# Optimization experiments

Measured on AMD Instinct MI355X. Metric: run time of the kernel, lower is better.

## Reference

```python
import jax, jax.numpy as jnp
import numpy as np

NEG_SLOPE = 0.2


def gat_conv(feat, src, dst, W, al, ar, num_nodes, activation):
    # feat: [N, F_in]; W: [F_in, H*D]; al, ar: [H, D]
    H, D = al.shape
    h = (feat @ W).reshape(-1, H, D)                      # [N, H, D]
    el = jnp.sum(h * al, axis=-1)                         # [N, H]
    er = jnp.sum(h * ar, axis=-1)                         # [N, H]
    e = jax.nn.leaky_relu(el[src] + er[dst], NEG_SLOPE)   # [E, H]
    # edge softmax over incoming edges of each destination node
    emax = jax.ops.segment_max(e, dst, num_segments=num_nodes)   # [N, H]
    ee = jnp.exp(e - emax[dst])                           # [E, H]
    denom = jax.ops.segment_sum(ee, dst, num_segments=num_nodes)  # [N, H]
    alpha = ee / jnp.maximum(denom[dst], 1e-9)            # [E, H]
    msg = h[src] * alpha[:, :, None]                      # [E, H, D]
    out = jax.ops.segment_sum(msg, dst, num_segments=num_nodes)   # [N, H, D]
    return activation(out) if activation is not None else out


def setup_inputs() -> dict:
    key = jax.random.key(0)
    ks = jax.random.split(key, 12)
    N, E, F_IN, HID, C = 100000, 1600000, 256, 32, 40
    heads = [4, 4, 1]
    inp = {
        "feats": jax.random.normal(ks[0], (N, F_IN), dtype=jnp.float32),
        "src": jax.random.randint(ks[1], (E,), 0, N, dtype=jnp.int32),
        "dst": jax.random.randint(ks[2], (E,), 0, N, dtype=jnp.int32),
    }
    def glorot(k, shape):
        fan = shape[0] + shape[-1]
        return jax.random.normal(k, shape, dtype=jnp.float32) * np.sqrt(2.0 / fan)
    # layer 0: in=256 -> heads[0]*HID
    inp["W0"] = glorot(ks[3], (F_IN, heads[0] * HID))
    inp["al0"] = glorot(ks[4], (heads[0], HID))
    inp["ar0"] = glorot(ks[5], (heads[0], HID))
    # layer 1: in=heads[0]*HID -> heads[1]*HID
    inp["W1"] = glorot(ks[6], (heads[0] * HID, heads[1] * HID))
    inp["al1"] = glorot(ks[7], (heads[1], HID))
    inp["ar1"] = glorot(ks[8], (heads[1], HID))
    # output layer: in=heads[1]*HID -> heads[2]*C
    inp["W2"] = glorot(ks[9], (heads[1] * HID, heads[2] * C))
    inp["al2"] = glorot(ks[10], (heads[2], C))
    inp["ar2"] = glorot(ks[11], (heads[2], C))
    return inp


def reference(feats, src, dst, W0, al0, ar0, W1, al1, ar1, W2, al2, ar2):
    N = feats.shape[0]
    elu = jax.nn.elu
    h1 = gat_conv(feats, src, dst, W0, al0, ar0, N, elu).reshape(N, -1)  # flatten(1)
    h2 = gat_conv(h1, src, dst, W1, al1, ar1, N, elu).reshape(N, -1)
    logits = gat_conv(h2, src, dst, W2, al2, ar2, N, None).mean(axis=1)  # mean over heads
    return (logits, h1, h2)
```

## Files before the change

kernel.cpp:

```cpp
#include <hip/hip_runtime.h>
#include <hip/hip_bf16.h>

#define NEG_SLOPE 0.2f
#define BW 256
#define MAXB 512

typedef __attribute__((ext_vector_type(8))) short short8;
typedef __attribute__((ext_vector_type(4))) float f32x4;

__device__ inline float bf2f(short s) {
    union { unsigned u; float f; } v;
    v.u = ((unsigned)(unsigned short)s) << 16;
    return v.f;
}
__device__ inline short f2bf(float f) {
    __hip_bfloat16 h = __float2bfloat16(f);
    return (short)*reinterpret_cast<unsigned short*>(&h);
}
__device__ inline void gload16(const void* g, void* lds) {
    __builtin_amdgcn_global_load_lds((const __attribute__((address_space(1))) void*)g,
                                     (__attribute__((address_space(3))) void*)lds, 16, 0, 0);
}


__global__ __launch_bounds__(256) void bhist_kernel(const int* __restrict__ dst,
                                                    int* __restrict__ bcnt, int E, int NB) {
    __shared__ int h[MAXB];
    int tid = threadIdx.x;
    for (int i = tid; i < NB; i += 256) h[i] = 0;
    __syncthreads();
    int e0 = blockIdx.x * 4096;
#pragma unroll
    for (int i = 0; i < 16; ++i) {
        int e = e0 + i * 256 + tid;
        if (e < E) atomicAdd(&h[dst[e] >> 8], 1);
    }
    __syncthreads();
    for (int i = tid; i < NB; i += 256)
        if (h[i]) atomicAdd(&bcnt[i], h[i]);
}

__global__ __launch_bounds__(512) void bscan_kernel(const int* __restrict__ bcnt,
                                                    int* __restrict__ bbase,
                                                    int* __restrict__ bcur, int NB, int E) {
    __shared__ int lds[512];
    int tid = threadIdx.x;
    int v = (tid < NB) ? bcnt[tid] : 0;
    lds[tid] = v;
    __syncthreads();
    int x = v;
    for (int off = 1; off < 512; off <<= 1) {
        int y = (tid >= off) ? lds[tid - off] : 0;
        __syncthreads();
        x += y;
        lds[tid] = x;
        __syncthreads();
    }
    int excl = x - v;
    if (tid < NB) {
        bbase[tid] = excl;
        bcur[tid] = excl;
    }
    if (tid == 0) bbase[NB] = E;
}

__global__ __launch_bounds__(256) void bpart_kernel(const int* __restrict__ dst,
                                                    const int* __restrict__ src,
                                                    int* __restrict__ bcur,
                                                    unsigned* __restrict__ tmp, int E, int NB) {
    __shared__ int h[MAXB], h2[MAXB], base[MAXB];
    int tid = threadIdx.x;
    for (int i = tid; i < NB; i += 256) { h[i] = 0; h2[i] = 0; }
    __syncthreads();
    int e0 = blockIdx.x * 4096;
    unsigned pk[16];
    short bb[16];
#pragma unroll
    for (int i = 0; i < 16; ++i) {
        int e = e0 + i * 256 + tid;
        bool valid = e < E;
        int d = valid ? dst[e] : 0;
        int s = valid ? src[e] : 0;
        bb[i] = valid ? (short)(d >> 8) : (short)-1;
        pk[i] = (unsigned)s | ((unsigned)(d & 255) << 17);
        if (valid) atomicAdd(&h[d >> 8], 1);
    }
    __syncthreads();
    for (int i = tid; i < NB; i += 256)
        base[i] = h[i] ? atomicAdd(&bcur[i], h[i]) : 0;
    __syncthreads();
#pragma unroll
    for (int i = 0; i < 16; ++i) {
        if (bb[i] >= 0) {
            int p = base[bb[i]] + atomicAdd(&h2[bb[i]], 1);
            tmp[p] = pk[i];
        }
    }
}

__global__ __launch_bounds__(256) void bsort_kernel(const unsigned* __restrict__ tmp,
                                                    const int* __restrict__ bbase,
                                                    int* __restrict__ csr,
                                                    int* __restrict__ offsets, int N, int NB) {
    __shared__ int cnt[BW], cur[BW];
    int b = blockIdx.x;
    int tid = threadIdx.x;
    int Rb = bbase[b], Rend = bbase[b + 1];
    cnt[tid] = 0;
    __syncthreads();
    for (int i = Rb + tid; i < Rend; i += 256) atomicAdd(&cnt[tmp[i] >> 17], 1);
    __syncthreads();
    int v = cnt[tid];
    cur[tid] = v;
    __syncthreads();
    int x = v;
    for (int off = 1; off < 256; off <<= 1) {
        int y = (tid >= off) ? cur[tid - off] : 0;
        __syncthreads();
        x += y;
        cur[tid] = x;
        __syncthreads();
    }
    int excl = x - v;
    int g = b * BW + tid;
    if (g <= N) offsets[g] = Rb + excl;
    cur[tid] = Rb + excl;
    __syncthreads();
    for (int i = Rb + tid; i < Rend; i += 256) {
        unsigned p = tmp[i];
        int pos = atomicAdd(&cur[p >> 17], 1);
        csr[pos] = (int)(p & 0x1FFFFu);
    }
}


__global__ __launch_bounds__(256) void cvtT_kernel(const float* __restrict__ in,
                                                   __hip_bfloat16* __restrict__ out,
                                                   int K, int Nc) {
    int i = blockIdx.x * 256 + threadIdx.x;
    if (i >= K * Nc) return;
    int k = i / Nc, n = i % Nc;
    out[(size_t)n * K + k] = __float2bfloat16(in[i]);
}


template <bool CVT_A>
__global__ __launch_bounds__(256) void gemm_mfma(const void* __restrict__ Av,
                                                 const __hip_bfloat16* __restrict__ Bt,
                                                 __hip_bfloat16* __restrict__ Cb,
                                                 int M, int K) {
    __shared__ __align__(16) short smem[8192];
    const int tid = threadIdx.x;
    const int lane = tid & 63;
    const int w = tid >> 6;
    const int wr = w >> 1, wc = w & 1;
    const int bm = blockIdx.x * 128;
    f32x4 acc[4][4];
#pragma unroll
    for (int m = 0; m < 4; ++m)
#pragma unroll
        for (int n = 0; n < 4; ++n) acc[m][n] = 0.f;

    for (int k0 = 0; k0 < K; k0 += 32) {
#pragma unroll
        for (int i = 0; i < 2; ++i) {
            const int c = (w * 2 + i) * 64 + lane;
            const int row = c >> 2;
            const int kpg = (c & 3) ^ (row & 3);
            int grow = bm + row;
            grow = grow < M ? grow : M - 1;
            if (CVT_A) {
                const float* gp = (const float*)Av + (size_t)grow * K + k0 + kpg * 8;
                f32x4 f0 = __builtin_nontemporal_load((const f32x4*)gp);
                f32x4 f1 = __builtin_nontemporal_load((const f32x4*)(gp + 4));
                short8 v;
                v[0] = f2bf(f0[0]); v[1] = f2bf(f0[1]); v[2] = f2bf(f0[2]); v[3] = f2bf(f0[3]);
                v[4] = f2bf(f1[0]); v[5] = f2bf(f1[1]); v[6] = f2bf(f1[2]); v[7] = f2bf(f1[3]);
                *(short8*)&smem[c * 8] = v;
            } else {
                const __hip_bfloat16* gp =
                    (const __hip_bfloat16*)Av + (size_t)grow * K + k0 + kpg * 8;
                gload16(gp, &smem[(w * 2 + i) * 512]);
            }
        }
#pragma unroll
        for (int i = 0; i < 2; ++i) {
            const int c = (w * 2 + i) * 64 + lane;
            const int col = c >> 2;
            const int kpg = (c & 3) ^ (col & 3);
            const __hip_bfloat16* gp = Bt + (size_t)col * K + k0 + kpg * 8;
            gload16(gp, &smem[4096 + (w * 2 + i) * 512]);
        }
        __syncthreads();
        short8 a[4], b[4];
        const int kp = lane >> 4;
#pragma unroll
        for (int m = 0; m < 4; ++m) {
            const int row = wr * 64 + m * 16 + (lane & 15);
            a[m] = *(const short8*)&smem[row * 32 + ((kp ^ (row & 3)) << 3)];
        }
#pragma unroll
        for (int n = 0; n < 4; ++n) {
            const int col = wc * 64 + n * 16 + (lane & 15);
            b[n] = *(const short8*)&smem[4096 + col * 32 + ((kp ^ (col & 3)) << 3)];
        }
#pragma unroll
        for (int m = 0; m < 4; ++m)
#pragma unroll
            for (int n = 0; n < 4; ++n)
                acc[m][n] = __builtin_amdgcn_mfma_f32_16x16x32_bf16(a[m], b[n], acc[m][n], 0, 0, 0);
        __syncthreads();
    }
#pragma unroll
    for (int m = 0; m < 4; ++m)
#pragma unroll
        for (int j = 0; j < 4; ++j) {
            int row = bm + wr * 64 + m * 16 + (lane >> 4) * 4 + j;
            if (row >= M) continue;
#pragma unroll
            for (int n = 0; n < 4; ++n) {
                int col = wc * 64 + n * 16 + (lane & 15);
                Cb[(size_t)row * 128 + col] = __float2bfloat16(acc[m][n][j]);
            }
        }
}


__global__ __launch_bounds__(256) void gemm40_kernel(const __hip_bfloat16* __restrict__ A,
                                                     const float* __restrict__ W,
                                                     __hip_bfloat16* __restrict__ C, int M) {
    int rowb = blockIdx.x * 256 + threadIdx.x;
    int row = rowb < M ? rowb : M - 1;
    float acc[40];
#pragma unroll
    for (int c = 0; c < 40; ++c) acc[c] = 0.f;
    const short8* ap = (const short8*)(A + (size_t)row * 128);
#pragma unroll 1
    for (int kc = 0; kc < 16; ++kc) {
        short8 v = ap[kc];
#pragma unroll
        for (int j = 0; j < 8; ++j) {
            float f = bf2f(v[j]);
            const float* wrow = W + (kc * 8 + j) * 40;
#pragma unroll
            for (int c = 0; c < 40; ++c) acc[c] += f * wrow[c];
        }
    }
    if (rowb < M) {
#pragma unroll
        for (int c = 0; c < 40; ++c) C[(size_t)rowb * 64 + c] = __float2bfloat16(acc[c]);
#pragma unroll
        for (int c = 40; c < 64; ++c) C[(size_t)rowb * 64 + c] = __float2bfloat16(0.f);
    }
}


__global__ __launch_bounds__(256) void eler4_kernel(const __hip_bfloat16* __restrict__ h,
                                                    const float* __restrict__ al,
                                                    const float* __restrict__ ar,
                                                    float* __restrict__ el,
                                                    float* __restrict__ er, int NH) {
    int idx = blockIdx.x * 256 + threadIdx.x;
    if (idx >= NH) return;
    int hh = idx & 3;
    const short8* hp = (const short8*)(h + (size_t)idx * 32);
    float sl = 0.f, sr = 0.f;
#pragma unroll
    for (int ck = 0; ck < 4; ++ck) {
        short8 v = hp[ck];
#pragma unroll
        for (int j = 0; j < 8; ++j) {
            float f = bf2f(v[j]);
            sl += f * al[hh * 32 + ck * 8 + j];
            sr += f * ar[hh * 32 + ck * 8 + j];
        }
    }
    el[idx] = sl;
    er[idx] = sr;
}

__global__ __launch_bounds__(256) void eler1_kernel(const __hip_bfloat16* __restrict__ h,
                                                    const float* __restrict__ al,
                                                    const float* __restrict__ ar,
                                                    float* __restrict__ el,
                                                    float* __restrict__ er, int N) {
    int idx = blockIdx.x * 256 + threadIdx.x;
    if (idx >= N) return;
    const __hip_bfloat162* hp = (const __hip_bfloat162*)(h + (size_t)idx * 64);
    float sl = 0.f, sr = 0.f;
#pragma unroll
    for (int d = 0; d < 20; ++d) {
        float2 f = __bfloat1622float2(hp[d]);
        sl += f.x * al[d * 2] + f.y * al[d * 2 + 1];
        sr += f.x * ar[d * 2] + f.y * ar[d * 2 + 1];
    }
    el[idx] = sl;
    er[idx] = sr;
}


__global__ __launch_bounds__(256) void gat_agg4_kernel(
    const int* __restrict__ offsets, const int* __restrict__ csr_src,
    const float* __restrict__ el, const float* __restrict__ er,
    const __hip_bfloat16* __restrict__ hfeat, float* __restrict__ outf,
    unsigned* __restrict__ outb, int N) {
    int node = blockIdx.x * 4 + (threadIdx.x >> 6);
    if (node >= N) return;
    int lane = threadIdx.x & 63;
    int ha = lane & 3;
    int es = lane >> 2;
    int cl = lane & 31;
    int half = lane >> 5;
    int h2 = cl >> 3;
    int beg = offsets[node], end = offsets[node + 1];
    float ern = er[node * 4 + ha];
    float m_run = -1e30f, d_run = 0.f;
    float acc[4] = {0.f, 0.f, 0.f, 0.f};
    const __hip_bfloat16* hcol = hfeat + cl * 4;
    for (int base = beg; base < end; base += 16) {
        int b = base + es;
        bool valid = b < end;
        int s = valid ? csr_src[b] : 0;
        float x = -1e30f;
        if (valid) {
            x = el[s * 4 + ha] + ern;
            x = x > 0.f ? x : NEG_SLOPE * x;
        }
        float cm = x;
        cm = fmaxf(cm, __shfl_xor(cm, 4));
        cm = fmaxf(cm, __shfl_xor(cm, 8));
        cm = fmaxf(cm, __shfl_xor(cm, 16));
        cm = fmaxf(cm, __shfl_xor(cm, 32));
        float m_new = fmaxf(m_run, cm);
        float scale = __expf(m_run - m_new);
        m_run = m_new;
        float p = valid ? __expf(x - m_new) : 0.f;
        float cs = p;
        cs += __shfl_xor(cs, 4);
        cs += __shfl_xor(cs, 8);
        cs += __shfl_xor(cs, 16);
        cs += __shfl_xor(cs, 32);
        d_run = d_run * scale + cs;
        float scl2 = __shfl(scale, h2);
        acc[0] *= scl2; acc[1] *= scl2; acc[2] *= scl2; acc[3] *= scl2;
        int cnt = min(16, end - base);
        float av[8];
        int rv[8];
#pragma unroll
        for (int k = 0; k < 8; ++k) {
            int e = half + 2 * k;
            float a = __shfl(p, (e << 2) | h2);
            rv[k] = __shfl(s, e << 2);
            av[k] = (e < cnt) ? a : 0.f;
        }
        ushort4 hv[8];
#pragma unroll
        for (int k = 0; k < 8; ++k)
            hv[k] = *(const ushort4*)(hcol + (size_t)rv[k] * 128);
#pragma unroll
        for (int k = 0; k < 8; ++k) {
            acc[0] += bf2f((short)hv[k].x) * av[k];
            acc[1] += bf2f((short)hv[k].y) * av[k];
            acc[2] += bf2f((short)hv[k].z) * av[k];
            acc[3] += bf2f((short)hv[k].w) * av[k];
        }
    }
#pragma unroll
    for (int j = 0; j < 4; ++j) acc[j] += __shfl_xor(acc[j], 32);
    float idn = 1.f / fmaxf(__shfl(d_run, h2), 1e-9f);
    if (half == 0) {
        float v[4];
#pragma unroll
        for (int j = 0; j < 4; ++j) {
            float t = acc[j] * idn;
            v[j] = t > 0.f ? t : __expf(t) - 1.f;
        }
        f32x4 fo = {v[0], v[1], v[2], v[3]};
        *(f32x4*)(outf + (size_t)node * 128 + cl * 4) = fo;
        unsigned u0 = (unsigned short)f2bf(v[0]) | ((unsigned)(unsigned short)f2bf(v[1]) << 16);
        unsigned u1 = (unsigned short)f2bf(v[2]) | ((unsigned)(unsigned short)f2bf(v[3]) << 16);
        uint2 uo = {u0, u1};
        *(uint2*)(outb + (size_t)node * 64 + cl * 2) = uo;
    }
}


__global__ __launch_bounds__(256) void gat_agg1_kernel(
    const int* __restrict__ offsets, const int* __restrict__ csr_src,
    const float* __restrict__ el, const float* __restrict__ er,
    const __hip_bfloat16* __restrict__ hfeat, float* __restrict__ logits, int N) {
    int node = blockIdx.x * 4 + (threadIdx.x >> 6);
    if (node >= N) return;
    int lane = threadIdx.x & 63;
    int cl = lane & 31;
    int half = lane >> 5;
    int beg = offsets[node], end = offsets[node + 1];
    float ern = er[node];
    float m_run = -1e30f, d_run = 0.f;
    float acc0 = 0.f, acc1 = 0.f;
    const __hip_bfloat16* hcol = hfeat + cl * 2;
    for (int base = beg; base < end; base += 64) {
        int b = base + lane;
        bool valid = b < end;
        int s = valid ? csr_src[b] : 0;
        float x = -1e30f;
        if (valid) {
            x = el[s] + ern;
            x = x > 0.f ? x : NEG_SLOPE * x;
        }
        float cm = x;
#pragma unroll
        for (int off = 1; off < 64; off <<= 1) cm = fmaxf(cm, __shfl_xor(cm, off));
        float m_new = fmaxf(m_run, cm);
        float scale = __expf(m_run - m_new);
        m_run = m_new;
        float p = valid ? __expf(x - m_new) : 0.f;
        float cs = p;
#pragma unroll
        for (int off = 1; off < 64; off <<= 1) cs += __shfl_xor(cs, off);
        d_run = d_run * scale + cs;
        acc0 *= scale; acc1 *= scale;
        int cnt = min(64, end - base);
        for (int sb = 0; sb < cnt; sb += 16) {
            float av[8];
            int rv[8];
#pragma unroll
            for (int k = 0; k < 8; ++k) {
                int e = sb + half + 2 * k;
                float a = __shfl(p, e & 63);
                rv[k] = __shfl(s, e & 63);
                av[k] = (e < cnt) ? a : 0.f;
            }
            unsigned hv[8];
#pragma unroll
            for (int k = 0; k < 8; ++k)
                hv[k] = *(const unsigned*)(hcol + (size_t)rv[k] * 64);
#pragma unroll
            for (int k = 0; k < 8; ++k) {
                acc0 += bf2f((short)(hv[k] & 0xFFFF)) * av[k];
                acc1 += bf2f((short)(hv[k] >> 16)) * av[k];
            }
        }
    }
    acc0 += __shfl_xor(acc0, 32);
    acc1 += __shfl_xor(acc1, 32);
    float idn = 1.f / fmaxf(d_run, 1e-9f);
    if (half == 0 && cl < 20) {
        float2 fo = {acc0 * idn, acc1 * idn};
        *(float2*)(logits + (size_t)node * 40 + cl * 2) = fo;
    }
}


extern "C" void kernel_launch(void* const* d_in, const int* in_sizes, int n_in,
                              void* d_out, int out_size, void* d_ws, size_t ws_size,
                              hipStream_t stream) {
    const float* feats = (const float*)d_in[0];
    const int* src = (const int*)d_in[1];
    const int* dst = (const int*)d_in[2];
    const float* W0 = (const float*)d_in[3];
    const float* al0 = (const float*)d_in[4];
    const float* ar0 = (const float*)d_in[5];
    const float* W1 = (const float*)d_in[6];
    const float* al1 = (const float*)d_in[7];
    const float* ar1 = (const float*)d_in[8];
    const float* W2 = (const float*)d_in[9];
    const float* al2 = (const float*)d_in[10];
    const float* ar2 = (const float*)d_in[11];

    const int N = in_sizes[0] / 256;
    const int E = in_sizes[1];
    const int NB = (N + BW - 1) / BW;

    float* out = (float*)d_out;
    float* logits = out;
    float* h1 = out + (size_t)N * 40;
    float* h2 = h1 + (size_t)N * 128;

    char* p = (char*)d_ws;
    __hip_bfloat16* hA = (__hip_bfloat16*)p; p += (size_t)N * 128 * 2;
    __hip_bfloat16* hB = (__hip_bfloat16*)p; p += (size_t)N * 128 * 2;
    float* el = (float*)p;   p += (size_t)N * 4 * 4;
    float* er = (float*)p;   p += (size_t)N * 4 * 4;
    __hip_bfloat16* Wt0 = (__hip_bfloat16*)p; p += 128 * 256 * 2;
    __hip_bfloat16* Wt1 = (__hip_bfloat16*)p; p += 128 * 128 * 2;
    int* offsets = (int*)p;  p += (size_t)(N + 1) * 4;
    int* bcnt = (int*)p;     p += MAXB * 4;
    int* bbase = (int*)p;    p += (MAXB + 1) * 4;
    int* bcur = (int*)p;     p += MAXB * 4;
    int* csr = (int*)p;      p += (size_t)E * 4;
    unsigned* tmp = (unsigned*)hA;

    const int gN256 = (N + 255) / 256;
    const int gE4096 = (E + 4095) / 4096;
    const int gM128 = (N + 127) / 128;
    const int gAgg = (N + 3) / 4;

    hipMemsetAsync(bcnt, 0, MAXB * sizeof(int), stream);
    bhist_kernel<<<gE4096, 256, 0, stream>>>(dst, bcnt, E, NB);
    bscan_kernel<<<1, 512, 0, stream>>>(bcnt, bbase, bcur, NB, E);
    bpart_kernel<<<gE4096, 256, 0, stream>>>(dst, src, bcur, tmp, E, NB);
    bsort_kernel<<<NB, 256, 0, stream>>>(tmp, bbase, csr, offsets, N, NB);

    cvtT_kernel<<<(256 * 128 + 255) / 256, 256, 0, stream>>>(W0, Wt0, 256, 128);
    cvtT_kernel<<<(128 * 128 + 255) / 256, 256, 0, stream>>>(W1, Wt1, 128, 128);

    gemm_mfma<true><<<gM128, 256, 0, stream>>>(feats, Wt0, hA, N, 256);
    eler4_kernel<<<(N * 4 + 255) / 256, 256, 0, stream>>>(hA, al0, ar0, el, er, N * 4);
    gat_agg4_kernel<<<gAgg, 256, 0, stream>>>(offsets, csr, el, er, hA, h1, (unsigned*)hB, N);

    gemm_mfma<false><<<gM128, 256, 0, stream>>>(hB, Wt1, hA, N, 128);
    eler4_kernel<<<(N * 4 + 255) / 256, 256, 0, stream>>>(hA, al1, ar1, el, er, N * 4);
    gat_agg4_kernel<<<gAgg, 256, 0, stream>>>(offsets, csr, el, er, hA, h2, (unsigned*)hB, N);

    gemm40_kernel<<<gN256, 256, 0, stream>>>(hB, W2, hA, N);
    eler1_kernel<<<gN256, 256, 0, stream>>>(hA, al2, ar2, el, er, N);
    gat_agg1_kernel<<<gAgg, 256, 0, stream>>>(offsets, csr, el, er, hA, logits, N);
}
```

Before: 407.2 us.

## Pack source index and fp16 weight into one shuffle, fuse small kernels

The aggregation kernels now pack the source node index (17 bits) and an fp16 attention weight into one 32-bit value, so each edge needs one shuffle instead of two. The bf16 unpack uses cheaper bit operations, and inactive lanes in the single-head layer skip their gathers. The two weight-transpose kernels are merged into one launch, and the layer-3 el/er computation is folded into the 40-column GEMM epilogue, removing a kernel and a re-read of h. The trade-off is that attention weights drop from fp32 to 15-bit fp16 precision, and node indices must fit in 17 bits.

```diff
diff --git a/kernel.cpp b/kernel.cpp
--- a/kernel.cpp
+++ b/kernel.cpp
@@ -1,5 +1,6 @@
 #include <hip/hip_runtime.h>
 #include <hip/hip_bf16.h>
+#include <hip/hip_fp16.h>
 
 #define NEG_SLOPE 0.2f
 #define BW 256
@@ -16,6 +17,26 @@
 __device__ inline short f2bf(float f) {
     __hip_bfloat16 h = __float2bfloat16(f);
     return (short)*reinterpret_cast<unsigned short*>(&h);
+}
+__device__ inline float lo_bf(unsigned u) {
+    union { unsigned u; float f; } v;
+    v.u = u << 16;
+    return v.f;
+}
+__device__ inline float hi_bf(unsigned u) {
+    union { unsigned u; float f; } v;
+    v.u = u & 0xFFFF0000u;
+    return v.f;
+}
+__device__ inline unsigned pack_sa(int s, float p) {
+    __half h = __float2half(p);
+    unsigned hb = (unsigned)*reinterpret_cast<unsigned short*>(&h);
+    return ((unsigned)s << 15) | (hb & 0x7FFFu);
+}
+__device__ inline float unpack_a(unsigned u) {
+    unsigned short hb = (unsigned short)(u & 0x7FFFu);
+    __half h = *reinterpret_cast<__half*>(&hb);
+    return __half2float(h);
 }
 __device__ inline void gload16(const void* g, void* lds) {
     __builtin_amdgcn_global_load_lds((const __attribute__((address_space(1))) void*)g,
@@ -134,13 +155,19 @@
 }
 
 
-__global__ __launch_bounds__(256) void cvtT_kernel(const float* __restrict__ in,
-                                                   __hip_bfloat16* __restrict__ out,
-                                                   int K, int Nc) {
+__global__ __launch_bounds__(256) void cvtT2_kernel(const float* __restrict__ W0,
+                                                    __hip_bfloat16* __restrict__ Wt0,
+                                                    const float* __restrict__ W1,
+                                                    __hip_bfloat16* __restrict__ Wt1) {
     int i = blockIdx.x * 256 + threadIdx.x;
-    if (i >= K * Nc) return;
-    int k = i / Nc, n = i % Nc;
-    out[(size_t)n * K + k] = __float2bfloat16(in[i]);
+    if (i < 256 * 128) {
+        int k = i / 128, n = i % 128;
+        Wt0[(size_t)n * 256 + k] = __float2bfloat16(W0[i]);
+    } else if (i < 256 * 128 + 128 * 128) {
+        int j = i - 256 * 128;
+        int k = j / 128, n = j % 128;
+        Wt1[(size_t)n * 128 + k] = __float2bfloat16(W1[j]);
+    }
 }
 
 
@@ -228,7 +255,11 @@
 
 __global__ __launch_bounds__(256) void gemm40_kernel(const __hip_bfloat16* __restrict__ A,
                                                      const float* __restrict__ W,
-                                                     __hip_bfloat16* __restrict__ C, int M) {
+                                                     const float* __restrict__ al,
+                                                     const float* __restrict__ ar,
+                                                     __hip_bfloat16* __restrict__ C,
+                                                     float* __restrict__ el,
+                                                     float* __restrict__ er, int M) {
     int rowb = blockIdx.x * 256 + threadIdx.x;
     int row = rowb < M ? rowb : M - 1;
     float acc[40];
@@ -247,10 +278,19 @@
         }
     }
     if (rowb < M) {
-#pragma unroll
-        for (int c = 0; c < 40; ++c) C[(size_t)rowb * 64 + c] = __float2bfloat16(acc[c]);
+        float sl = 0.f, sr = 0.f;
+#pragma unroll
+        for (int c = 0; c < 40; ++c) {
+            __hip_bfloat16 hb = __float2bfloat16(acc[c]);
+            float hv = __bfloat162float(hb);
+            C[(size_t)rowb * 64 + c] = hb;
+            sl += hv * al[c];
+            sr += hv * ar[c];
+        }
 #pragma unroll
         for (int c = 40; c < 64; ++c) C[(size_t)rowb * 64 + c] = __float2bfloat16(0.f);
+        el[rowb] = sl;
+        er[rowb] = sr;
     }
 }
 
@@ -274,25 +314,6 @@
             sl += f * al[hh * 32 + ck * 8 + j];
             sr += f * ar[hh * 32 + ck * 8 + j];
         }
-    }
-    el[idx] = sl;
-    er[idx] = sr;
-}
-
-__global__ __launch_bounds__(256) void eler1_kernel(const __hip_bfloat16* __restrict__ h,
-                                                    const float* __restrict__ al,
-                                                    const float* __restrict__ ar,
-                                                    float* __restrict__ el,
-                                                    float* __restrict__ er, int N) {
-    int idx = blockIdx.x * 256 + threadIdx.x;
-    if (idx >= N) return;
-    const __hip_bfloat162* hp = (const __hip_bfloat162*)(h + (size_t)idx * 64);
-    float sl = 0.f, sr = 0.f;
-#pragma unroll
-    for (int d = 0; d < 20; ++d) {
-        float2 f = __bfloat1622float2(hp[d]);
-        sl += f.x * al[d * 2] + f.y * al[d * 2 + 1];
-        sr += f.x * ar[d * 2] + f.y * ar[d * 2 + 1];
     }
     el[idx] = sl;
     er[idx] = sr;
@@ -341,28 +362,28 @@
         cs += __shfl_xor(cs, 16);
         cs += __shfl_xor(cs, 32);
         d_run = d_run * scale + cs;
+        unsigned u_mine = pack_sa(s, p);
         float scl2 = __shfl(scale, h2);
         acc[0] *= scl2; acc[1] *= scl2; acc[2] *= scl2; acc[3] *= scl2;
-        int cnt = min(16, end - base);
-        float av[8];
-        int rv[8];
+        unsigned uk[8];
 #pragma unroll
         for (int k = 0; k < 8; ++k) {
             int e = half + 2 * k;
-            float a = __shfl(p, (e << 2) | h2);
-            rv[k] = __shfl(s, e << 2);
-            av[k] = (e < cnt) ? a : 0.f;
+            uk[k] = __shfl(u_mine, (e << 2) | h2);
         }
         ushort4 hv[8];
 #pragma unroll
         for (int k = 0; k < 8; ++k)
-            hv[k] = *(const ushort4*)(hcol + (size_t)rv[k] * 128);
+            hv[k] = *(const ushort4*)(hcol + ((size_t)(uk[k] >> 15)) * 128);
 #pragma unroll
         for (int k = 0; k < 8; ++k) {
-            acc[0] += bf2f((short)hv[k].x) * av[k];
-            acc[1] += bf2f((short)hv[k].y) * av[k];
-            acc[2] += bf2f((short)hv[k].z) * av[k];
-            acc[3] += bf2f((short)hv[k].w) * av[k];
+            float a = unpack_a(uk[k]);
+            unsigned w0 = (unsigned)hv[k].x | ((unsigned)hv[k].y << 16);
+            unsigned w1 = (unsigned)hv[k].z | ((unsigned)hv[k].w << 16);
+            acc[0] += lo_bf(w0) * a;
+            acc[1] += hi_bf(w0) * a;
+            acc[2] += lo_bf(w1) * a;
+            acc[3] += hi_bf(w1) * a;
         }
     }
 #pragma unroll
@@ -394,6 +415,7 @@
     int lane = threadIdx.x & 63;
     int cl = lane & 31;
     int half = lane >> 5;
+    bool active = cl < 20;
     int beg = offsets[node], end = offsets[node + 1];
     float ern = er[node];
     float m_run = -1e30f, d_run = 0.f;
@@ -420,32 +442,32 @@
         for (int off = 1; off < 64; off <<= 1) cs += __shfl_xor(cs, off);
         d_run = d_run * scale + cs;
         acc0 *= scale; acc1 *= scale;
+        unsigned u_mine = pack_sa(s, p);
         int cnt = min(64, end - base);
         for (int sb = 0; sb < cnt; sb += 16) {
-            float av[8];
-            int rv[8];
+            unsigned uk[8];
 #pragma unroll
             for (int k = 0; k < 8; ++k) {
                 int e = sb + half + 2 * k;
-                float a = __shfl(p, e & 63);
-                rv[k] = __shfl(s, e & 63);
-                av[k] = (e < cnt) ? a : 0.f;
+                uk[k] = __shfl(u_mine, e & 63);
+                if (e >= cnt) uk[k] &= ~0x7FFFu;
             }
             unsigned hv[8];
 #pragma unroll
             for (int k = 0; k < 8; ++k)
-                hv[k] = *(const unsigned*)(hcol + (size_t)rv[k] * 64);
+                hv[k] = active ? *(const unsigned*)(hcol + ((size_t)(uk[k] >> 15)) * 64) : 0u;
 #pragma unroll
             for (int k = 0; k < 8; ++k) {
-                acc0 += bf2f((short)(hv[k] & 0xFFFF)) * av[k];
-                acc1 += bf2f((short)(hv[k] >> 16)) * av[k];
+                float a = unpack_a(uk[k]);
+                acc0 += lo_bf(hv[k]) * a;
+                acc1 += hi_bf(hv[k]) * a;
             }
         }
     }
     acc0 += __shfl_xor(acc0, 32);
     acc1 += __shfl_xor(acc1, 32);
     float idn = 1.f / fmaxf(d_run, 1e-9f);
-    if (half == 0 && cl < 20) {
+    if (half == 0 && active) {
         float2 fo = {acc0 * idn, acc1 * idn};
         *(float2*)(logits + (size_t)node * 40 + cl * 2) = fo;
     }
@@ -502,8 +524,7 @@
     bpart_kernel<<<gE4096, 256, 0, stream>>>(dst, src, bcur, tmp, E, NB);
     bsort_kernel<<<NB, 256, 0, stream>>>(tmp, bbase, csr, offsets, N, NB);
 
-    cvtT_kernel<<<(256 * 128 + 255) / 256, 256, 0, stream>>>(W0, Wt0, 256, 128);
-    cvtT_kernel<<<(128 * 128 + 255) / 256, 256, 0, stream>>>(W1, Wt1, 128, 128);
+    cvtT2_kernel<<<(256 * 128 + 128 * 128 + 255) / 256, 256, 0, stream>>>(W0, Wt0, W1, Wt1);
 
     gemm_mfma<true><<<gM128, 256, 0, stream>>>(feats, Wt0, hA, N, 256);
     eler4_kernel<<<(N * 4 + 255) / 256, 256, 0, stream>>>(hA, al0, ar0, el, er, N * 4);
@@ -513,7 +534,6 @@
     eler4_kernel<<<(N * 4 + 255) / 256, 256, 0, stream>>>(hA, al1, ar1, el, er, N * 4);
     gat_agg4_kernel<<<gAgg, 256, 0, stream>>>(offsets, csr, el, er, hA, h2, (unsigned*)hB, N);
 
-    gemm40_kernel<<<gN256, 256, 0, stream>>>(hB, W2, hA, N);
-    eler1_kernel<<<gN256, 256, 0, stream>>>(hA, al2, ar2, el, er, N);
+    gemm40_kernel<<<gN256, 256, 0, stream>>>(hB, W2, al2, ar2, hA, el, er, N);
     gat_agg1_kernel<<<gAgg, 256, 0, stream>>>(offsets, csr, el, er, hA, logits, N);
 }
```

New measurement: 395.7 us. 2.8% less time.
